# Performance work log

Measured on AMD Instinct MI355X. Metric: run time of the kernel, lower is better.

## Reference

```python
import jax, jax.numpy as jnp
import numpy as np

B, L, T_BASE = 8192, 512, 4
T = T_BASE + 2            # +START, +STOP
START, STOP = T_BASE, T_BASE + 1
NEG = -10000.0


def setup_inputs() -> dict:
    key = jax.random.key(0)
    k1, k2, k3, k4 = jax.random.split(key, 4)
    feats = jax.random.normal(k1, (B, L, T), dtype=jnp.float32)
    trans = jax.random.normal(k2, (T, T), dtype=jnp.float32)
    # transitions[START, :] = -10000 (never transition out of nothing into START... i.e. into START)
    trans = trans.at[START, :].set(NEG)
    # transitions[:, STOP] = -10000 (never transition from STOP)
    trans = trans.at[:, STOP].set(NEG)
    tags = jax.random.randint(k3, (B, L), 0, T_BASE, dtype=jnp.int64)
    seq_lengths = jax.random.randint(k4, (B,), 1, L + 1, dtype=jnp.int32)
    return {"feats": feats, "transitions": trans, "tags": tags, "seq_lengths": seq_lengths}


def _crf_nll(feats, trans, tags, seq_lengths):
    # feats: [B, L, T], trans: [T, T] with trans[next, prev], tags: [B, L], seq_lengths: [B]
    mask = (jnp.arange(L)[None, :] < seq_lengths[:, None])  # [B, L] bool

    # ---- forward algorithm (log partition), batched over B, scanned over time ----
    init_alpha = jnp.full((feats.shape[0], T), NEG, dtype=feats.dtype).at[:, START].set(0.0)

    def step(alpha, xs):
        feat_t, mask_t = xs  # [B, T], [B]
        # scores[b, next, prev] = alpha[b, prev] + trans[next, prev]
        scores = alpha[:, None, :] + trans[None, :, :]
        new_alpha = jax.nn.logsumexp(scores, axis=-1) + feat_t  # [B, T]
        alpha = jnp.where(mask_t[:, None], new_alpha, alpha)
        return alpha, None

    feats_t = jnp.swapaxes(feats, 0, 1)   # [L, B, T]
    mask_t = jnp.swapaxes(mask, 0, 1)     # [L, B]
    alpha, _ = jax.lax.scan(step, init_alpha, (feats_t, mask_t))
    log_z = jax.nn.logsumexp(alpha + trans[STOP][None, :], axis=-1)  # [B]

    # ---- gold path score, fully vectorized ----
    tags32 = tags.astype(jnp.int32)
    start_col = jnp.full((tags32.shape[0], 1), START, dtype=jnp.int32)
    tags_ext = jnp.concatenate([start_col, tags32], axis=1)  # [B, L+1]
    trans_sc = trans[tags_ext[:, 1:], tags_ext[:, :-1]]       # [B, L]
    emit_sc = jnp.take_along_axis(feats, tags32[..., None], axis=2)[..., 0]  # [B, L]
    maskf = mask.astype(feats.dtype)
    gold = jnp.sum(maskf * (trans_sc + emit_sc), axis=1)      # [B]
    last_tag = jnp.take_along_axis(tags32, (seq_lengths[:, None] - 1).astype(jnp.int32), axis=1)[:, 0]
    gold = gold + trans[STOP, last_tag]

    return jnp.sum(log_z - gold) / feats.shape[0]


def reference(feats, transitions, tags, seq_lengths):
    return _crf_nll(feats, transitions, tags, seq_lengths)
```

## Files before the change

### kernel.cpp

```cpp
#include <hip/hip_runtime.h>


#define BB 8192
#define LL 512
#define LN2F 0.69314718055994530942f

__device__ __forceinline__ float uniformf(float x) {
    return __uint_as_float(__builtin_amdgcn_readfirstlane(__float_as_uint(x)));
}

#define RENORM16(P, MEX)                                                \
  do {                                                                  \
    float m_ = fmaxf(P[0], P[1]);                                       \
    _Pragma("unroll") for (int z_ = 2; z_ < 16; ++z_) m_ = fmaxf(m_, P[z_]); \
    const int ee_ = (int)((__float_as_uint(m_) >> 23) & 255) - 127;     \
    const float sc_ = __uint_as_float((unsigned)(127 - ee_) << 23);     \
    _Pragma("unroll") for (int z_ = 0; z_ < 16; ++z_) P[z_] *= sc_;     \
    MEX += ee_;                                                         \
  } while (0)

#define STEP(R, F0, F1, F2, F3)                                         \
  do {                                                                  \
    const bool act_ = (base + (R)) < len;                               \
    const float f0_=(F0), f1_=(F1), f2_=(F2), f3_=(F3);                 \
    const float fe0_=__expf(f0_), fe1_=__expf(f1_);                     \
    const float fe2_=__expf(f2_), fe3_=__expf(f3_);                     \
    _Pragma("unroll")                                                   \
    for (int j = 0; j < 4; ++j) {                                       \
      const float c0_=P[0*4+j], c1_=P[1*4+j], c2_=P[2*4+j], c3_=P[3*4+j]; \
      const float t0_ = fmaf(E[0], c0_, fmaf(E[1], c1_, fmaf(E[2], c2_, E[3] *c3_))); \
      const float t1_ = fmaf(E[4], c0_, fmaf(E[5], c1_, fmaf(E[6], c2_, E[7] *c3_))); \
      const float t2_ = fmaf(E[8], c0_, fmaf(E[9], c1_, fmaf(E[10],c2_, E[11]*c3_))); \
      const float t3_ = fmaf(E[12],c0_, fmaf(E[13],c1_, fmaf(E[14],c2_, E[15]*c3_))); \
      P[0*4+j] = act_ ? fe0_*t0_ : P[0*4+j];                            \
      P[1*4+j] = act_ ? fe1_*t1_ : P[1*4+j];                            \
      P[2*4+j] = act_ ? fe2_*t2_ : P[2*4+j];                            \
      P[3*4+j] = act_ ? fe3_*t3_ : P[3*4+j];                            \
    }                                                                   \
    const int tg_ = tg##R;                                              \
    const float lut_ = sT[tg_ * 6 + tgp##R];                            \
    const float em_  = (tg_ & 2) ? ((tg_ & 1) ? f3_ : f2_)              \
                                 : ((tg_ & 1) ? f1_ : f0_);             \
    gold += act_ ? (lut_ + em_) : 0.f;                                  \
  } while (0)

__global__ __launch_bounds__(128, 8) void crf_tree(
    const float* __restrict__ feats,
    const float* __restrict__ trans,
    const int*   __restrict__ tags,
    const int*   __restrict__ lens,
    float* __restrict__ partials)
{
    __shared__ float sT[36];

    const int tid  = threadIdx.x;
    const int lane = tid & 63;
    const int wv   = tid >> 6;
    const int b    = blockIdx.x * 2 + wv;

    if (tid < 36) sT[tid] = trans[tid];
    __syncthreads();

    float E[16], e4[4], e5[4];
    #pragma unroll
    for (int i = 0; i < 16; ++i)
        E[i] = uniformf(__expf(sT[(i >> 2) * 6 + (i & 3)]));
    #pragma unroll
    for (int i = 0; i < 4; ++i) {
        e4[i] = uniformf(__expf(sT[i * 6 + 4]));
        e5[i] = uniformf(__expf(sT[30 + i]));
    }

    const int len  = lens[b];
    const int base = lane * 8;
    const bool lane0 = (lane == 0);

    const float* fp = feats + (size_t)b * (LL * 6) + lane * 48;
    const float4 A0 = *(const float4*)(fp + 0);
    const float2 A1 = *(const float2*)(fp + 6);
    const float2 A2 = *(const float2*)(fp + 8);
    const float4 B0 = *(const float4*)(fp + 12);
    const float2 B1 = *(const float2*)(fp + 18);
    const float2 B2 = *(const float2*)(fp + 20);
    const float4 C0 = *(const float4*)(fp + 24);
    const float2 C1 = *(const float2*)(fp + 30);
    const float2 C2 = *(const float2*)(fp + 32);
    const float4 D0 = *(const float4*)(fp + 36);
    const float2 D1 = *(const float2*)(fp + 42);
    const float2 D2 = *(const float2*)(fp + 44);

    const int* tbp = tags + (size_t)b * LL + base;
    const int4 ta  = *(const int4*)tbp;
    const int4 tb4 = *(const int4*)(tbp + 4);
    const int tg0=ta.x&3,  tg1=ta.y&3,  tg2=ta.z&3,  tg3=ta.w&3;
    const int tg4=tb4.x&3, tg5=tb4.y&3, tg6=tb4.z&3, tg7=tb4.w&3;
    const int ptail = __shfl_up(tg7, 1, 64);
    const int prev0 = lane0 ? 4 : ptail;
    const int tgp1=tg0, tgp2=tg1, tgp3=tg2,
              tgp4=tg3, tgp5=tg4, tgp6=tg5, tgp7=tg6;

    float P[16];
    #pragma unroll
    for (int z = 0; z < 16; ++z) P[z] = (z % 5 == 0) ? 1.f : 0.f;
    int   mex  = 0;
    float gold = 0.f;

    {
        const bool act_ = base < len;
        const float f0_=A0.x, f1_=A0.y, f2_=A0.z, f3_=A0.w;
        const float fe0_=__expf(f0_), fe1_=__expf(f1_);
        const float fe2_=__expf(f2_), fe3_=__expf(f3_);
        #pragma unroll
        for (int j = 0; j < 4; ++j) {
            const float t0_ = lane0 ? e4[0] : E[0*4+j];
            const float t1_ = lane0 ? e4[1] : E[1*4+j];
            const float t2_ = lane0 ? e4[2] : E[2*4+j];
            const float t3_ = lane0 ? e4[3] : E[3*4+j];
            P[0*4+j] = act_ ? fe0_*t0_ : P[0*4+j];
            P[1*4+j] = act_ ? fe1_*t1_ : P[1*4+j];
            P[2*4+j] = act_ ? fe2_*t2_ : P[2*4+j];
            P[3*4+j] = act_ ? fe3_*t3_ : P[3*4+j];
        }
        const float lut_ = sT[tg0 * 6 + prev0];
        const float em_  = (tg0 & 2) ? ((tg0 & 1) ? f3_ : f2_)
                                     : ((tg0 & 1) ? f1_ : f0_);
        gold += act_ ? (lut_ + em_) : 0.f;
    }
    STEP(1, A1.x, A1.y, A2.x, A2.y);
    STEP(2, B0.x, B0.y, B0.z, B0.w);
    STEP(3, B1.x, B1.y, B2.x, B2.y);
    RENORM16(P, mex);
    STEP(4, C0.x, C0.y, C0.z, C0.w);
    STEP(5, C1.x, C1.y, C2.x, C2.y);
    STEP(6, D0.x, D0.y, D0.z, D0.w);
    STEP(7, D1.x, D1.y, D2.x, D2.y);
    RENORM16(P, mex);

    {
        const unsigned dl = (unsigned)(len - 1 - base);
        if (dl < 8u) gold += sT[30 + (tbp[dl] & 3)];
    }

    #pragma unroll
    for (int k = 1; k <= 32; k <<= 1) {
        float Q[16];
        #pragma unroll
        for (int z = 0; z < 16; ++z) Q[z] = __shfl_down(P[z], k, 64);
        const int mq = __shfl_down(mex, k, 64);
        float N[16];
        #pragma unroll
        for (int i = 0; i < 4; ++i)
            #pragma unroll
            for (int j = 0; j < 4; ++j)
                N[i*4+j] = fmaf(Q[i*4+0], P[0*4+j], fmaf(Q[i*4+1], P[1*4+j],
                           fmaf(Q[i*4+2], P[2*4+j], Q[i*4+3] * P[3*4+j])));
        #pragma unroll
        for (int z = 0; z < 16; ++z) P[z] = N[z];
        mex += mq;
        if (k <= 8) RENORM16(P, mex);
    }

    #pragma unroll
    for (int k = 1; k <= 32; k <<= 1)
        gold += __shfl_xor(gold, k, 64);

    const float dot = fmaf(e5[0], P[0], fmaf(e5[1], P[4],
                      fmaf(e5[2], P[8], e5[3] * P[12])));
    const float logz = fmaf((float)mex, LN2F, __logf(dot));
    if (lane == 0)
        partials[b] = logz - gold;
}

__global__ __launch_bounds__(256) void k_reduce(const float* __restrict__ partials,
                                               float* __restrict__ out)
{
    __shared__ float sh[256];
    const int t = threadIdx.x;
    float s = 0.f;
    #pragma unroll
    for (int j = 0; j < 32; ++j) s += partials[t + 256 * j];
    sh[t] = s;
    __syncthreads();
    #pragma unroll
    for (int d = 128; d > 0; d >>= 1) {
        if (t < d) sh[t] += sh[t + d];
        __syncthreads();
    }
    if (t == 0) out[0] = sh[0] * (1.0f / 8192.0f);
}

extern "C" void kernel_launch(void* const* d_in, const int* in_sizes, int n_in,
                              void* d_out, int out_size, void* d_ws, size_t ws_size,
                              hipStream_t stream) {
    const float* feats = (const float*)d_in[0];
    const float* trans = (const float*)d_in[1];
    const int*   tags  = (const int*)d_in[2];
    const int*   lens  = (const int*)d_in[3];
    float* out = (float*)d_out;
    float* partials = (float*)d_ws;

    crf_tree<<<BB / 2, 128, 0, stream>>>(feats, trans, tags, lens, partials);
    k_reduce<<<1, 256, 0, stream>>>(partials, out);
}
```

Before: 37.48 us.

## Split each sequence across 16 lanes with 32-step chunks to shrink shuffle tree

Each wavefront now handles four sequences, with 16 lanes per sequence, and each lane processes 32 timesteps sequentially in a loop of 4-step chunks instead of 8 timesteps. The cross-lane 4x4 matrix product tree drops from 6 levels to 4, which cuts shuffle and matmul overhead per sequence. The cost is longer serial per-lane dependency chains and strided per-lane loads that coalesce less well. Block size changes to 256 with different launch bounds.

```diff
diff --git a/kernel.cpp b/kernel.cpp
--- a/kernel.cpp
+++ b/kernel.cpp
@@ -19,9 +19,9 @@
     MEX += ee_;                                                         \
   } while (0)
 
-#define STEP(R, F0, F1, F2, F3)                                         \
+#define STEP(ABS, F0, F1, F2, F3, TG, PV)                               \
   do {                                                                  \
-    const bool act_ = (base + (R)) < len;                               \
+    const bool act_ = (ABS) < len;                                      \
     const float f0_=(F0), f1_=(F1), f2_=(F2), f3_=(F3);                 \
     const float fe0_=__expf(f0_), fe1_=__expf(f1_);                     \
     const float fe2_=__expf(f2_), fe3_=__expf(f3_);                     \
@@ -37,14 +37,13 @@
       P[2*4+j] = act_ ? fe2_*t2_ : P[2*4+j];                            \
       P[3*4+j] = act_ ? fe3_*t3_ : P[3*4+j];                            \
     }                                                                   \
-    const int tg_ = tg##R;                                              \
-    const float lut_ = sT[tg_ * 6 + tgp##R];                            \
-    const float em_  = (tg_ & 2) ? ((tg_ & 1) ? f3_ : f2_)              \
-                                 : ((tg_ & 1) ? f1_ : f0_);             \
+    const float lut_ = sT[(TG) * 6 + (PV)];                             \
+    const float em_  = ((TG) & 2) ? (((TG) & 1) ? f3_ : f2_)            \
+                                  : (((TG) & 1) ? f1_ : f0_);           \
     gold += act_ ? (lut_ + em_) : 0.f;                                  \
   } while (0)
 
-__global__ __launch_bounds__(128, 8) void crf_tree(
+__global__ __launch_bounds__(256, 2) void crf_tree(
     const float* __restrict__ feats,
     const float* __restrict__ trans,
     const int*   __restrict__ tags,
@@ -56,7 +55,9 @@
     const int tid  = threadIdx.x;
     const int lane = tid & 63;
     const int wv   = tid >> 6;
-    const int b    = blockIdx.x * 2 + wv;
+    const int g    = lane >> 4;
+    const int c    = lane & 15;
+    const int b    = blockIdx.x * 16 + wv * 4 + g;
 
     if (tid < 36) sT[tid] = trans[tid];
     __syncthreads();
@@ -72,81 +73,88 @@
     }
 
     const int len  = lens[b];
-    const int base = lane * 8;
-    const bool lane0 = (lane == 0);
-
-    const float* fp = feats + (size_t)b * (LL * 6) + lane * 48;
-    const float4 A0 = *(const float4*)(fp + 0);
-    const float2 A1 = *(const float2*)(fp + 6);
-    const float2 A2 = *(const float2*)(fp + 8);
-    const float4 B0 = *(const float4*)(fp + 12);
-    const float2 B1 = *(const float2*)(fp + 18);
-    const float2 B2 = *(const float2*)(fp + 20);
-    const float4 C0 = *(const float4*)(fp + 24);
-    const float2 C1 = *(const float2*)(fp + 30);
-    const float2 C2 = *(const float2*)(fp + 32);
-    const float4 D0 = *(const float4*)(fp + 36);
-    const float2 D1 = *(const float2*)(fp + 42);
-    const float2 D2 = *(const float2*)(fp + 44);
-
-    const int* tbp = tags + (size_t)b * LL + base;
-    const int4 ta  = *(const int4*)tbp;
-    const int4 tb4 = *(const int4*)(tbp + 4);
-    const int tg0=ta.x&3,  tg1=ta.y&3,  tg2=ta.z&3,  tg3=ta.w&3;
-    const int tg4=tb4.x&3, tg5=tb4.y&3, tg6=tb4.z&3, tg7=tb4.w&3;
-    const int ptail = __shfl_up(tg7, 1, 64);
-    const int prev0 = lane0 ? 4 : ptail;
-    const int tgp1=tg0, tgp2=tg1, tgp3=tg2,
-              tgp4=tg3, tgp5=tg4, tgp6=tg5, tgp7=tg6;
+    const int base = c * 32;
+    const bool seg0 = (c == 0);
+
+    const float* fp  = feats + (size_t)b * (LL * 6) + (size_t)base * 6;
+    const int*   tbp = tags  + (size_t)b * LL + base;
+
+    const int pv0 = seg0 ? 4 : (tbp[-1] & 3);
 
     float P[16];
     #pragma unroll
     for (int z = 0; z < 16; ++z) P[z] = (z % 5 == 0) ? 1.f : 0.f;
     int   mex  = 0;
     float gold = 0.f;
+    int   pv;
 
     {
-        const bool act_ = base < len;
-        const float f0_=A0.x, f1_=A0.y, f2_=A0.z, f3_=A0.w;
-        const float fe0_=__expf(f0_), fe1_=__expf(f1_);
-        const float fe2_=__expf(f2_), fe3_=__expf(f3_);
-        #pragma unroll
-        for (int j = 0; j < 4; ++j) {
-            const float t0_ = lane0 ? e4[0] : E[0*4+j];
-            const float t1_ = lane0 ? e4[1] : E[1*4+j];
-            const float t2_ = lane0 ? e4[2] : E[2*4+j];
-            const float t3_ = lane0 ? e4[3] : E[3*4+j];
-            P[0*4+j] = act_ ? fe0_*t0_ : P[0*4+j];
-            P[1*4+j] = act_ ? fe1_*t1_ : P[1*4+j];
-            P[2*4+j] = act_ ? fe2_*t2_ : P[2*4+j];
-            P[3*4+j] = act_ ? fe3_*t3_ : P[3*4+j];
+        const int4 tq = *(const int4*)tbp;
+        const int t0 = tq.x & 3, t1 = tq.y & 3, t2 = tq.z & 3, t3 = tq.w & 3;
+        const float4 a0 = *(const float4*)(fp + 0);
+        const float2 a1 = *(const float2*)(fp + 6);
+        const float2 a2 = *(const float2*)(fp + 8);
+        const float4 b0 = *(const float4*)(fp + 12);
+        const float2 b1 = *(const float2*)(fp + 18);
+        const float2 b2 = *(const float2*)(fp + 20);
+        {
+            const bool act_ = base < len;
+            const float f0_=a0.x, f1_=a0.y, f2_=a0.z, f3_=a0.w;
+            const float fe0_=__expf(f0_), fe1_=__expf(f1_);
+            const float fe2_=__expf(f2_), fe3_=__expf(f3_);
+            #pragma unroll
+            for (int j = 0; j < 4; ++j) {
+                const float u0 = seg0 ? e4[0] : E[0*4+j];
+                const float u1 = seg0 ? e4[1] : E[1*4+j];
+                const float u2 = seg0 ? e4[2] : E[2*4+j];
+                const float u3 = seg0 ? e4[3] : E[3*4+j];
+                P[0*4+j] = act_ ? fe0_*u0 : P[0*4+j];
+                P[1*4+j] = act_ ? fe1_*u1 : P[1*4+j];
+                P[2*4+j] = act_ ? fe2_*u2 : P[2*4+j];
+                P[3*4+j] = act_ ? fe3_*u3 : P[3*4+j];
+            }
+            const float lut_ = sT[t0 * 6 + pv0];
+            const float em_  = (t0 & 2) ? ((t0 & 1) ? f3_ : f2_)
+                                        : ((t0 & 1) ? f1_ : f0_);
+            gold += act_ ? (lut_ + em_) : 0.f;
         }
-        const float lut_ = sT[tg0 * 6 + prev0];
-        const float em_  = (tg0 & 2) ? ((tg0 & 1) ? f3_ : f2_)
-                                     : ((tg0 & 1) ? f1_ : f0_);
-        gold += act_ ? (lut_ + em_) : 0.f;
-    }
-    STEP(1, A1.x, A1.y, A2.x, A2.y);
-    STEP(2, B0.x, B0.y, B0.z, B0.w);
-    STEP(3, B1.x, B1.y, B2.x, B2.y);
-    RENORM16(P, mex);
-    STEP(4, C0.x, C0.y, C0.z, C0.w);
-    STEP(5, C1.x, C1.y, C2.x, C2.y);
-    STEP(6, D0.x, D0.y, D0.z, D0.w);
-    STEP(7, D1.x, D1.y, D2.x, D2.y);
-    RENORM16(P, mex);
+        STEP(base+1, a1.x, a1.y, a2.x, a2.y, t1, t0);
+        STEP(base+2, b0.x, b0.y, b0.z, b0.w, t2, t1);
+        STEP(base+3, b1.x, b1.y, b2.x, b2.y, t3, t2);
+        RENORM16(P, mex);
+        pv = t3;
+    }
+
+    for (int p = 1; p < 8; ++p) {
+        const int4 tq = *(const int4*)(tbp + p * 4);
+        const int t0 = tq.x & 3, t1 = tq.y & 3, t2 = tq.z & 3, t3 = tq.w & 3;
+        const float* q = fp + p * 24;
+        const float4 a0 = *(const float4*)(q + 0);
+        const float2 a1 = *(const float2*)(q + 6);
+        const float2 a2 = *(const float2*)(q + 8);
+        const float4 b0 = *(const float4*)(q + 12);
+        const float2 b1 = *(const float2*)(q + 18);
+        const float2 b2 = *(const float2*)(q + 20);
+        const int s0 = base + p * 4;
+        STEP(s0+0, a0.x, a0.y, a0.z, a0.w, t0, pv);
+        STEP(s0+1, a1.x, a1.y, a2.x, a2.y, t1, t0);
+        STEP(s0+2, b0.x, b0.y, b0.z, b0.w, t2, t1);
+        STEP(s0+3, b1.x, b1.y, b2.x, b2.y, t3, t2);
+        RENORM16(P, mex);
+        pv = t3;
+    }
 
     {
         const unsigned dl = (unsigned)(len - 1 - base);
-        if (dl < 8u) gold += sT[30 + (tbp[dl] & 3)];
-    }
-
-    #pragma unroll
-    for (int k = 1; k <= 32; k <<= 1) {
+        if (dl < 32u) gold += sT[30 + (tbp[dl] & 3)];
+    }
+
+    #pragma unroll
+    for (int k = 1; k <= 8; k <<= 1) {
         float Q[16];
         #pragma unroll
-        for (int z = 0; z < 16; ++z) Q[z] = __shfl_down(P[z], k, 64);
-        const int mq = __shfl_down(mex, k, 64);
+        for (int z = 0; z < 16; ++z) Q[z] = __shfl_down(P[z], k, 16);
+        const int mq = __shfl_down(mex, k, 16);
         float N[16];
         #pragma unroll
         for (int i = 0; i < 4; ++i)
@@ -157,17 +165,17 @@
         #pragma unroll
         for (int z = 0; z < 16; ++z) P[z] = N[z];
         mex += mq;
-        if (k <= 8) RENORM16(P, mex);
-    }
-
-    #pragma unroll
-    for (int k = 1; k <= 32; k <<= 1)
-        gold += __shfl_xor(gold, k, 64);
+        RENORM16(P, mex);
+    }
+
+    #pragma unroll
+    for (int k = 1; k <= 8; k <<= 1)
+        gold += __shfl_xor(gold, k, 16);
 
     const float dot = fmaf(e5[0], P[0], fmaf(e5[1], P[4],
                       fmaf(e5[2], P[8], e5[3] * P[12])));
     const float logz = fmaf((float)mex, LN2F, __logf(dot));
-    if (lane == 0)
+    if (c == 0)
         partials[b] = logz - gold;
 }
 
@@ -199,6 +207,6 @@
     float* out = (float*)d_out;
     float* partials = (float*)d_ws;
 
-    crf_tree<<<BB / 2, 128, 0, stream>>>(feats, trans, tags, lens, partials);
+    crf_tree<<<BB / 16, 256, 0, stream>>>(feats, trans, tags, lens, partials);
     k_reduce<<<1, 256, 0, stream>>>(partials, out);
 }
```

Result: slower. 46.24 us (+23.4%).
